# Kernel optimization log

Measured on AMD Instinct MI355X. Metric: run time of the kernel, lower is better.

The kernel has to match this reference:

```python
import jax, jax.numpy as jnp
import numpy as np


def _maxpool3d(x, win):
    # x: (B, C, D, H, W); SAME padding via w//2 on each spatial side, stride 1
    pads = [(0, 0), (0, 0)] + [(w // 2, w // 2) for w in win]
    return jax.lax.reduce_window(x, -jnp.inf, jax.lax.max,
                                 (1, 1) + tuple(win), (1, 1, 1, 1, 1), pads)


def _soft_skeletonize(x, thresh_width=5):
    # Iterative morphological erosion: x <- relu(x - relu(maxpool(minpool(x)) - minpool(x)))
    for _ in range(thresh_width):
        p1 = -_maxpool3d(-x, (3, 1, 1))  # directional min-pool along D
        p2 = -_maxpool3d(-x, (1, 3, 1))  # along H
        p3 = -_maxpool3d(-x, (1, 1, 3))  # along W
        min_pool = jnp.minimum(jnp.minimum(p1, p2), p3)
        contour = jax.nn.relu(_maxpool3d(min_pool, (3, 3, 3)) - min_pool)
        x = jax.nn.relu(x - contour)
    return x


def _positive_intersection(center_line, vessel):
    B, C = center_line.shape[0], center_line.shape[1]
    clf = center_line.reshape(B, C, -1)
    vf = vessel.reshape(B, C, -1)
    intersection = jnp.sum(clf * vf, axis=-1).sum(0)          # (C,)
    return (intersection + 1e-12) / (jnp.sum(clf, axis=-1).sum(0) + 1e-12)


def setup_inputs() -> dict:
    key = jax.random.key(0)
    k1, k2 = jax.random.split(key)
    B, C, D, H, W = 2, 1, 64, 256, 256
    logits = jax.random.normal(k1, (B, C, D, H, W), dtype=jnp.float32)
    target = jax.random.uniform(k2, (B, C, D, H, W), dtype=jnp.float32)
    mask = jnp.ones((B, C, D, H, W), dtype=jnp.float32)
    return {"logits": logits, "target": target, "mask": mask}


def reference(logits, target, mask):
    THRESH_WIDTH = 5
    pred = jax.nn.sigmoid(logits) * mask
    tgt = target * mask
    target_skeleton = _soft_skeletonize(tgt, THRESH_WIDTH)
    cl_pred = _soft_skeletonize(pred, THRESH_WIDTH)
    clrecall = _positive_intersection(target_skeleton, pred)[0]
    clacc = _positive_intersection(cl_pred, tgt)[0]
    cldice = 2.0 * clrecall * clacc / (clrecall + clacc + 1e-12)
    return 1.0 - cldice
```

## Files before the change

kernel.cpp:

```cpp
#include <hip/hip_runtime.h>
#include <math.h>


constexpr int Bn = 2;
constexpr int D  = 64;
constexpr int H  = 256;
constexpr int W  = 256;
constexpr int HW = H * W;
constexpr int NV = Bn * D * H * W;

constexpr int CD  = 16;
constexpr int XSF = 76;
constexpr int XPQ = 768;
constexpr int RSF = 68;

__device__ __forceinline__ void seg_barrier_v0() {
    asm volatile("s_waitcnt vmcnt(0) lgkmcnt(0)" ::: "memory");
    __builtin_amdgcn_s_barrier();
    asm volatile("" ::: "memory");
}
__device__ __forceinline__ void seg_barrier_v2() {
    asm volatile("s_waitcnt vmcnt(2) lgkmcnt(0)" ::: "memory");
    __builtin_amdgcn_s_barrier();
    asm volatile("" ::: "memory");
}

__device__ __forceinline__ float4 vmin4(float4 a, float4 b) {
    return make_float4(fminf(a.x,b.x), fminf(a.y,b.y), fminf(a.z,b.z), fminf(a.w,b.w));
}
__device__ __forceinline__ float4 vmax4(float4 a, float4 b) {
    return make_float4(fmaxf(a.x,b.x), fmaxf(a.y,b.y), fmaxf(a.z,b.z), fmaxf(a.w,b.w));
}
__device__ __forceinline__ float4 sh1(float4 a, float4 b) { return make_float4(a.y,a.z,a.w,b.x); }
__device__ __forceinline__ float4 sh3(float4 a, float4 b) { return make_float4(a.w,b.x,b.y,b.z); }

__global__ __launch_bounds__(256) void prep_kernel(const float* __restrict__ logits,
                                                   const float* __restrict__ target,
                                                   const float* __restrict__ mask,
                                                   float* __restrict__ pred,
                                                   float* __restrict__ tgt,
                                                   float* __restrict__ infbuf) {
    int i = (blockIdx.x * 256 + threadIdx.x) * 4;
    float4 lg = *(const float4*)(logits + i);
    float4 tg = *(const float4*)(target + i);
    float4 mk = *(const float4*)(mask + i);
    float4 p, t;
    p.x = (1.0f/(1.0f+expf(-lg.x)))*mk.x;  t.x = tg.x*mk.x;
    p.y = (1.0f/(1.0f+expf(-lg.y)))*mk.y;  t.y = tg.y*mk.y;
    p.z = (1.0f/(1.0f+expf(-lg.z)))*mk.z;  t.z = tg.z*mk.z;
    p.w = (1.0f/(1.0f+expf(-lg.w)))*mk.w;  t.w = tg.w*mk.w;
    *(float4*)(pred + i) = p;
    *(float4*)(tgt + i)  = t;
    if (blockIdx.x == 0 && threadIdx.x == 0) {
        *(float4*)infbuf = make_float4(INFINITY, INFINITY, INFINITY, INFINITY);
    }
}

template <bool FINAL>
__global__ __launch_bounds__(256) void skel_iter_kernel(
        const float* __restrict__ in0, float* __restrict__ out0,
        const float* __restrict__ oth0, double* __restrict__ acc0,
        const float* __restrict__ in1, float* __restrict__ out1,
        const float* __restrict__ oth1, double* __restrict__ acc1,
        const float* __restrict__ infbuf) {
    __shared__ float sx[4][XPQ * 4];
    __shared__ float srm[2][34 * RSF];

    int cpx = gridDim.x >> 3;
    int hwb = blockIdx.x;
    int bx  = (hwb & 7) * cpx + (hwb >> 3);

    int t   = bx >> 8;
    int bt  = bx & 255;
    int w0  = (bt & 3) * 64;
    int h0  = ((bt >> 2) & 7) * 32;
    int gd0 = ((bt >> 5) & 3) * CD;
    int b   = (bt >> 7) & 1;

    const float* xin  = t ? in1  : in0;
    float*       xout = t ? out1 : out0;
    const float* oth  = t ? oth1 : oth0;
    double*      accp = t ? acc1 : acc0;

    int tid  = threadIdx.x;
    int r    = tid >> 3;
    int k    = tid & 7;
    int wv   = tid >> 6;
    int lane = tid & 63;

    const float* xb  = xin + b * (D * HW);
    float*       ob  = xout ? (xout + b * (D * HW)) : nullptr;
    const float* otb = oth + b * (D * HW);

    const float4 INF4  = make_float4( INFINITY,  INFINITY,  INFINITY,  INFINITY);
    const float4 NINF4 = make_float4(-INFINITY, -INFINITY, -INFINITY, -INFINITY);

    int  offe[3];
    bool okl[3];
    for (int i = 0; i < 3; ++i) {
        int c = wv + 4 * i;
        int j = 64 * c + lane;
        int row = j / 19;
        int q = j - 19 * row;
        int gh = h0 - 2 + row;
        int gw = w0 - 4 + 4 * q;
        okl[i] = (q < 18) && (row < 36) &&
                 ((unsigned)gh < (unsigned)H) && ((unsigned)gw < (unsigned)W);
        offe[i] = gh * W + gw;
    }

    auto issue_g = [&](int p) {
        bool pok = (p >= 0 && p < D);
        const float* pbase = xb + (long)p * HW;
        float* slot = sx[(p + 4) & 3];
        #pragma unroll
        for (int i = 0; i < 3; ++i) {
            const float* src = (pok && okl[i]) ? (pbase + offe[i]) : infbuf;
            float* dst = slot + (wv + 4 * i) * 256;
            __builtin_amdgcn_global_load_lds(
                (const __attribute__((address_space(1))) void*)src,
                (__attribute__((address_space(3))) void*)dst, 16, 0, 0);
        }
    };

    issue_g(gd0 - 2); issue_g(gd0 - 1); issue_g(gd0); issue_g(gd0 + 1);
    __syncthreads();

    float4 h1lo=NINF4, h1hi=NINF4, h2lo=NINF4, h2hi=NINF4;
    float4 p1lo=NINF4, p1hi=NINF4, p2lo=NINF4, p2hi=NINF4;
    float4 rmplo=NINF4, rmphi=NINF4;
    float4 xplo=INF4, xphi=INF4;
    double s0 = 0.0, s1 = 0.0;

    for (int s = gd0 - 1; s <= gd0 + CD + 1; ++s) {
        if (s >= gd0 && s + 2 <= gd0 + CD + 1) issue_g(s + 2);
        asm volatile("" ::: "memory");

        bool sv = (s >= 0 && s < D && s <= gd0 + CD);
        float4 lo = NINF4, hi = NINF4, rmlo = NINF4, rmhi = NINF4;
        float4 vM1 = INF4, vM2 = INF4;
        if (sv) {
            const float* xq = sx[(s + 4) & 3];
            const float* xm = sx[(s + 3) & 3];
            const float* xp = sx[(s + 5) & 3];
            {
                const float* rc  = &xq[(r + 2) * XSF + 8 * k];
                const float* ru  = &xq[(r + 1) * XSF + 8 * k];
                const float* rd  = &xq[(r + 3) * XSF + 8 * k];
                const float* rm_ = &xm[(r + 2) * XSF + 8 * k];
                const float* rp_ = &xp[(r + 2) * XSF + 8 * k];
                float4 X0 = *(const float4*)rc,        X1 = *(const float4*)(rc + 4),
                       X2 = *(const float4*)(rc + 8),  X3 = *(const float4*)(rc + 12);
                float4 U1 = *(const float4*)(ru + 4),  U2 = *(const float4*)(ru + 8);
                float4 Dn1= *(const float4*)(rd + 4),  Dn2= *(const float4*)(rd + 8);
                float4 M1 = *(const float4*)(rm_ + 4), M2 = *(const float4*)(rm_ + 8);
                float4 P1 = *(const float4*)(rp_ + 4), P2 = *(const float4*)(rp_ + 8);
                vM1 = M1; vM2 = M2;
                lo = vmin4(vmin4(sh3(X0, X1), X1), sh1(X1, X2));
                lo = vmin4(lo, vmin4(vmin4(U1, Dn1), vmin4(M1, P1)));
                hi = vmin4(vmin4(sh3(X1, X2), X2), sh1(X2, X3));
                hi = vmin4(hi, vmin4(vmin4(U2, Dn2), vmin4(M2, P2)));
                float eL = __shfl_up(hi.w, 1);
                float eR = __shfl_down(lo.x, 1);
                if (k == 0) {
                    eL = -INFINITY;
                    if (w0 > 0) {
                        float w3 = fminf(fminf(X0.z, X0.w), X1.x);
                        eL = fminf(fminf(w3, fminf(ru[3], rd[3])),
                                   fminf(rm_[3], rp_[3]));
                    }
                }
                if (k == 7) {
                    eR = -INFINITY;
                    if (w0 + 64 < W) {
                        float w3 = fminf(fminf(X2.w, X3.x), X3.y);
                        eR = fminf(fminf(w3, fminf(ru[12], rd[12])),
                                   fminf(rm_[12], rp_[12]));
                    }
                }
                rmlo = vmax4(vmax4(make_float4(eL, lo.x, lo.y, lo.z), lo),
                             make_float4(lo.y, lo.z, lo.w, hi.x));
                rmhi = vmax4(vmax4(make_float4(lo.w, hi.x, hi.y, hi.z), hi),
                             make_float4(hi.y, hi.z, hi.w, eR));
                float* rw = &srm[s & 1][(r + 1) * RSF + 8 * k];
                *(float4*)rw       = rmlo;
                *(float4*)(rw + 4) = rmhi;
            }
            if (tid < 16) {
                int mr2 = (tid >> 3) ? 33 : 0;
                int k2  = tid & 7;
                int gh2 = h0 - 1 + mr2;
                float4 hlo = NINF4, hhi = NINF4;
                if ((unsigned)gh2 < (unsigned)H) {
                    int xr2 = mr2 + 1;
                    const float* rc  = &xq[xr2 * XSF + 8 * k2];
                    const float* ru  = &xq[(xr2 - 1) * XSF + 8 * k2];
                    const float* rd  = &xq[(xr2 + 1) * XSF + 8 * k2];
                    const float* rm_ = &xm[xr2 * XSF + 8 * k2];
                    const float* rp_ = &xp[xr2 * XSF + 8 * k2];
                    float4 X0 = *(const float4*)rc,        X1 = *(const float4*)(rc + 4),
                           X2 = *(const float4*)(rc + 8),  X3 = *(const float4*)(rc + 12);
                    float4 U1 = *(const float4*)(ru + 4),  U2 = *(const float4*)(ru + 8);
                    float4 Dn1= *(const float4*)(rd + 4),  Dn2= *(const float4*)(rd + 8);
                    float4 M1 = *(const float4*)(rm_ + 4), M2 = *(const float4*)(rm_ + 8);
                    float4 P1 = *(const float4*)(rp_ + 4), P2 = *(const float4*)(rp_ + 8);
                    float4 l2 = vmin4(vmin4(sh3(X0, X1), X1), sh1(X1, X2));
                    l2 = vmin4(l2, vmin4(vmin4(U1, Dn1), vmin4(M1, P1)));
                    float4 g2 = vmin4(vmin4(sh3(X1, X2), X2), sh1(X2, X3));
                    g2 = vmin4(g2, vmin4(vmin4(U2, Dn2), vmin4(M2, P2)));
                    float eL2 = -INFINITY, eR2 = -INFINITY;
                    if (w0 + 8 * k2 - 1 >= 0) {
                        float w3 = fminf(fminf(X0.z, X0.w), X1.x);
                        eL2 = fminf(fminf(w3, fminf(ru[3], rd[3])),
                                    fminf(rm_[3], rp_[3]));
                    }
                    if (w0 + 8 * k2 + 8 < W) {
                        float w3 = fminf(fminf(X2.w, X3.x), X3.y);
                        eR2 = fminf(fminf(w3, fminf(ru[12], rd[12])),
                                    fminf(rm_[12], rp_[12]));
                    }
                    hlo = vmax4(vmax4(make_float4(eL2, l2.x, l2.y, l2.z), l2),
                                make_float4(l2.y, l2.z, l2.w, g2.x));
                    hhi = vmax4(vmax4(make_float4(l2.w, g2.x, g2.y, g2.z), g2),
                                make_float4(g2.y, g2.z, g2.w, eR2));
                }
                float* hw = &srm[s & 1][mr2 * RSF + 8 * k2];
                *(float4*)hw       = hlo;
                *(float4*)(hw + 4) = hhi;
            }
        }

        int dm = s - 1;
        float4 xclo = INF4, xchi = INF4;
        if (dm >= gd0 && dm <= gd0 + CD - 1) {
            if (sv) { xclo = vM1; xchi = vM2; }
            else {
                const float* xd = sx[(dm + 4) & 3];
                xclo = *(const float4*)&xd[(r + 2) * XSF + 8 * k + 4];
                xchi = *(const float4*)&xd[(r + 2) * XSF + 8 * k + 8];
            }
        }

        float4 hclo = NINF4, hchi = NINF4;
        if (s >= gd0 && dm >= 0 && dm < D) {
            const float* m = srm[dm & 1];
            float4 a0 = *(const float4*)&m[r * RSF + 8 * k];
            float4 a1 = *(const float4*)&m[r * RSF + 8 * k + 4];
            float4 b0 = *(const float4*)&m[(r + 2) * RSF + 8 * k];
            float4 b1 = *(const float4*)&m[(r + 2) * RSF + 8 * k + 4];
            hclo = vmax4(vmax4(a0, rmplo), b0);
            hchi = vmax4(vmax4(a1, rmphi), b1);
        }

        int d = s - 2;
        if (d >= gd0 && d <= gd0 + CD - 1) {
            float4 mxlo = vmax4(h2lo, vmax4(h1lo, hclo));
            float4 mxhi = vmax4(h2hi, vmax4(h1hi, hchi));
            float4 rlo, rhi;
            rlo.x = fmaxf(xplo.x - (mxlo.x - p2lo.x), 0.0f);
            rlo.y = fmaxf(xplo.y - (mxlo.y - p2lo.y), 0.0f);
            rlo.z = fmaxf(xplo.z - (mxlo.z - p2lo.z), 0.0f);
            rlo.w = fmaxf(xplo.w - (mxlo.w - p2lo.w), 0.0f);
            rhi.x = fmaxf(xphi.x - (mxhi.x - p2hi.x), 0.0f);
            rhi.y = fmaxf(xphi.y - (mxhi.y - p2hi.y), 0.0f);
            rhi.z = fmaxf(xphi.z - (mxhi.z - p2hi.z), 0.0f);
            rhi.w = fmaxf(xphi.w - (mxhi.w - p2hi.w), 0.0f);
            long off = (long)d * HW + (h0 + r) * W + (w0 + 8 * k);
            if constexpr (FINAL) {
                float4 o1 = *(const float4*)(otb + off);
                float4 o2 = *(const float4*)(otb + off + 4);
                s0 += (double)(rlo.x * o1.x) + (double)(rlo.y * o1.y)
                    + (double)(rlo.z * o1.z) + (double)(rlo.w * o1.w)
                    + (double)(rhi.x * o2.x) + (double)(rhi.y * o2.y)
                    + (double)(rhi.z * o2.z) + (double)(rhi.w * o2.w);
                s1 += (double)rlo.x + (double)rlo.y + (double)rlo.z + (double)rlo.w
                    + (double)rhi.x + (double)rhi.y + (double)rhi.z + (double)rhi.w;
            } else {
                *(float4*)(ob + off)     = rlo;
                *(float4*)(ob + off + 4) = rhi;
            }
        }

        h2lo = h1lo; h2hi = h1hi; h1lo = hclo; h1hi = hchi;
        p2lo = p1lo; p2hi = p1hi; p1lo = lo;   p1hi = hi;
        rmplo = rmlo; rmphi = rmhi;
        xplo = xclo;  xphi = xchi;

        if (s <= gd0 + 1) seg_barrier_v0();
        else              seg_barrier_v2();
    }

    if constexpr (FINAL) {
        for (int off = 32; off > 0; off >>= 1) {
            s0 += __shfl_down(s0, off, 64);
            s1 += __shfl_down(s1, off, 64);
        }
        if ((tid & 63) == 0) {
            atomicAdd(&accp[0], s0);
            atomicAdd(&accp[1], s1);
        }
    }
}

__global__ void final_kernel(const double* __restrict__ acc, float* __restrict__ out) {
    double clrecall = (acc[0] + 1e-12) / (acc[1] + 1e-12);
    double clacc    = (acc[2] + 1e-12) / (acc[3] + 1e-12);
    double cldice   = 2.0 * clrecall * clacc / (clrecall + clacc + 1e-12);
    out[0] = (float)(1.0 - cldice);
}

extern "C" void kernel_launch(void* const* d_in, const int* in_sizes, int n_in,
                              void* d_out, int out_size, void* d_ws, size_t ws_size,
                              hipStream_t stream) {
    const float* logits = (const float*)d_in[0];
    const float* target = (const float*)d_in[1];
    const float* mask   = (const float*)d_in[2];
    float* out = (float*)d_out;

    float* pred = (float*)d_ws;
    float* tgt  = pred + NV;
    float* A0   = tgt + NV;
    float* B0   = A0 + NV;

    bool big = ws_size >= (size_t)6 * NV * 4 + 64;
    float* A1    = big ? (B0 + NV) : A0;
    float* B1    = big ? (A1 + NV) : B0;
    double* acc  = big ? (double*)(B1 + NV) : (double*)(B0 + NV);
    float* infb  = (float*)(acc + 4);

    hipMemsetAsync(acc, 0, 4 * sizeof(double), stream);

    dim3 blk(256);
    prep_kernel<<<dim3(NV / 1024), blk, 0, stream>>>(logits, target, mask, pred, tgt, infb);

    if (big) {
        dim3 g(512);
        skel_iter_kernel<false><<<g, blk, 0, stream>>>(tgt, A0, pred, acc, pred, A1, tgt, acc + 2, infb);
        skel_iter_kernel<false><<<g, blk, 0, stream>>>(A0, B0, pred, acc, A1, B1, tgt, acc + 2, infb);
        skel_iter_kernel<false><<<g, blk, 0, stream>>>(B0, A0, pred, acc, B1, A1, tgt, acc + 2, infb);
        skel_iter_kernel<false><<<g, blk, 0, stream>>>(A0, B0, pred, acc, A1, B1, tgt, acc + 2, infb);
        skel_iter_kernel<true ><<<g, blk, 0, stream>>>(B0, nullptr, pred, acc, B1, nullptr, tgt, acc + 2, infb);
    } else {
        dim3 g(256);
        skel_iter_kernel<false><<<g, blk, 0, stream>>>(tgt, A0, pred, acc, tgt, A0, pred, acc, infb);
        skel_iter_kernel<false><<<g, blk, 0, stream>>>(A0, B0, pred, acc, A0, B0, pred, acc, infb);
        skel_iter_kernel<false><<<g, blk, 0, stream>>>(B0, A0, pred, acc, B0, A0, pred, acc, infb);
        skel_iter_kernel<false><<<g, blk, 0, stream>>>(A0, B0, pred, acc, A0, B0, pred, acc, infb);
        skel_iter_kernel<true ><<<g, blk, 0, stream>>>(B0, nullptr, pred, acc, B0, nullptr, pred, acc, infb);
        skel_iter_kernel<false><<<g, blk, 0, stream>>>(pred, A0, tgt, acc + 2, pred, A0, tgt, acc + 2, infb);
        skel_iter_kernel<false><<<g, blk, 0, stream>>>(A0, B0, tgt, acc + 2, A0, B0, tgt, acc + 2, infb);
        skel_iter_kernel<false><<<g, blk, 0, stream>>>(B0, A0, tgt, acc + 2, B0, A0, tgt, acc + 2, infb);
        skel_iter_kernel<false><<<g, blk, 0, stream>>>(A0, B0, tgt, acc + 2, A0, B0, tgt, acc + 2, infb);
        skel_iter_kernel<true ><<<g, blk, 0, stream>>>(B0, nullptr, tgt, acc + 2, B0, nullptr, tgt, acc + 2, infb);
    }

    final_kernel<<<1, 1, 0, stream>>>(acc, out);
}
```

Measured before the change: 282.7 us.

## Fuse sigmoid/mask prep into first and final skeleton iteration kernels

Removes the separate prep kernel and the pred/tgt intermediate buffers. The first skeletonization pass now loads logits/target and mask through registers, applies sigmoid and masking, and writes the result to LDS with a register-prefetch pipeline in place of async global-to-LDS loads. The final pass recomputes pred or tgt on the fly for the intersection sums. This cuts a full read/write sweep of the volume and one launch, but the first pass loses the asynchronous LDS load path and recomputes sigmoid on halo elements.

```diff
diff --git a/kernel.cpp b/kernel.cpp
--- a/kernel.cpp
+++ b/kernel.cpp
@@ -24,6 +24,11 @@
     __builtin_amdgcn_s_barrier();
     asm volatile("" ::: "memory");
 }
+__device__ __forceinline__ void seg_barrier_lgkm() {
+    asm volatile("s_waitcnt lgkmcnt(0)" ::: "memory");
+    __builtin_amdgcn_s_barrier();
+    asm volatile("" ::: "memory");
+}
 
 __device__ __forceinline__ float4 vmin4(float4 a, float4 b) {
     return make_float4(fminf(a.x,b.x), fminf(a.y,b.y), fminf(a.z,b.z), fminf(a.w,b.w));
@@ -34,34 +39,31 @@
 __device__ __forceinline__ float4 sh1(float4 a, float4 b) { return make_float4(a.y,a.z,a.w,b.x); }
 __device__ __forceinline__ float4 sh3(float4 a, float4 b) { return make_float4(a.w,b.x,b.y,b.z); }
 
-__global__ __launch_bounds__(256) void prep_kernel(const float* __restrict__ logits,
-                                                   const float* __restrict__ target,
-                                                   const float* __restrict__ mask,
-                                                   float* __restrict__ pred,
-                                                   float* __restrict__ tgt,
-                                                   float* __restrict__ infbuf) {
-    int i = (blockIdx.x * 256 + threadIdx.x) * 4;
-    float4 lg = *(const float4*)(logits + i);
-    float4 tg = *(const float4*)(target + i);
-    float4 mk = *(const float4*)(mask + i);
-    float4 p, t;
-    p.x = (1.0f/(1.0f+expf(-lg.x)))*mk.x;  t.x = tg.x*mk.x;
-    p.y = (1.0f/(1.0f+expf(-lg.y)))*mk.y;  t.y = tg.y*mk.y;
-    p.z = (1.0f/(1.0f+expf(-lg.z)))*mk.z;  t.z = tg.z*mk.z;
-    p.w = (1.0f/(1.0f+expf(-lg.w)))*mk.w;  t.w = tg.w*mk.w;
-    *(float4*)(pred + i) = p;
-    *(float4*)(tgt + i)  = t;
-    if (blockIdx.x == 0 && threadIdx.x == 0) {
-        *(float4*)infbuf = make_float4(INFINITY, INFINITY, INFINITY, INFINITY);
-    }
-}
-
-template <bool FINAL>
+__device__ __forceinline__ float4 apply_mode(float4 a, const float* __restrict__ pm,
+                                             long ix, int mode) {
+    if (mode != 0) {
+        if (mode == 2) {
+            a.x = 1.0f / (1.0f + expf(-a.x));
+            a.y = 1.0f / (1.0f + expf(-a.y));
+            a.z = 1.0f / (1.0f + expf(-a.z));
+            a.w = 1.0f / (1.0f + expf(-a.w));
+        }
+        float4 m = *(const float4*)(pm + ix);
+        a.x *= m.x; a.y *= m.y; a.z *= m.z; a.w *= m.w;
+    }
+    return a;
+}
+
+template <bool FINAL, int IM0, int IM1, int OM0, int OM1>
 __global__ __launch_bounds__(256) void skel_iter_kernel(
-        const float* __restrict__ in0, float* __restrict__ out0,
-        const float* __restrict__ oth0, double* __restrict__ acc0,
-        const float* __restrict__ in1, float* __restrict__ out1,
-        const float* __restrict__ oth1, double* __restrict__ acc1,
+        const float* __restrict__ iA0, const float* __restrict__ iB0,
+        float* __restrict__ out0,
+        const float* __restrict__ oA0, const float* __restrict__ oB0,
+        double* __restrict__ acc0,
+        const float* __restrict__ iA1, const float* __restrict__ iB1,
+        float* __restrict__ out1,
+        const float* __restrict__ oA1, const float* __restrict__ oB1,
+        double* __restrict__ acc1,
         const float* __restrict__ infbuf) {
     __shared__ float sx[4][XPQ * 4];
     __shared__ float srm[2][34 * RSF];
@@ -77,10 +79,14 @@
     int gd0 = ((bt >> 5) & 3) * CD;
     int b   = (bt >> 7) & 1;
 
-    const float* xin  = t ? in1  : in0;
-    float*       xout = t ? out1 : out0;
-    const float* oth  = t ? oth1 : oth0;
-    double*      accp = t ? acc1 : acc0;
+    const float* iA = t ? iA1 : iA0;
+    const float* iB = t ? iB1 : iB0;
+    const int    im = t ? IM1 : IM0;
+    float*     xout = t ? out1 : out0;
+    const float* oA = t ? oA1 : oA0;
+    const float* oB = t ? oB1 : oB0;
+    const int    om = t ? OM1 : OM0;
+    double*    accp = t ? acc1 : acc0;
 
     int tid  = threadIdx.x;
     int r    = tid >> 3;
@@ -88,9 +94,12 @@
     int wv   = tid >> 6;
     int lane = tid & 63;
 
-    const float* xb  = xin + b * (D * HW);
-    float*       ob  = xout ? (xout + b * (D * HW)) : nullptr;
-    const float* otb = oth + b * (D * HW);
+    long base = (long)b * (D * HW);
+    const float* xbA = iA + base;
+    const float* xbB = iB ? iB + base : nullptr;
+    float*       ob  = xout ? xout + base : nullptr;
+    const float* otA = oA ? oA + base : nullptr;
+    const float* otB = oB ? oB + base : nullptr;
 
     const float4 INF4  = make_float4( INFINITY,  INFINITY,  INFINITY,  INFINITY);
     const float4 NINF4 = make_float4(-INFINITY, -INFINITY, -INFINITY, -INFINITY);
@@ -111,7 +120,7 @@
 
     auto issue_g = [&](int p) {
         bool pok = (p >= 0 && p < D);
-        const float* pbase = xb + (long)p * HW;
+        const float* pbase = xbA + (long)p * HW;
         float* slot = sx[(p + 4) & 3];
         #pragma unroll
         for (int i = 0; i < 3; ++i) {
@@ -123,7 +132,38 @@
         }
     };
 
-    issue_g(gd0 - 2); issue_g(gd0 - 1); issue_g(gd0); issue_g(gd0 + 1);
+    float4 Pa, Pb, Pc;
+    auto issue_r = [&](int p) {
+        if (p < 0 || p >= D) { Pa = Pb = Pc = INF4; return; }
+        const float* pA = xbA + (long)p * HW;
+        const float* pM = xbB ? xbB + (long)p * HW : nullptr;
+        float4 v[3];
+        #pragma unroll
+        for (int i = 0; i < 3; ++i) {
+            if (okl[i]) {
+                float4 a = *(const float4*)(pA + offe[i]);
+                v[i] = apply_mode(a, pM, offe[i], im);
+            } else {
+                v[i] = INF4;
+            }
+        }
+        Pa = v[0]; Pb = v[1]; Pc = v[2];
+    };
+    auto commit_r = [&](int p, float4 va, float4 vb, float4 vc) {
+        float* slot = sx[(p + 4) & 3];
+        *(float4*)&slot[(wv + 0) * 256 + 4 * lane] = va;
+        *(float4*)&slot[(wv + 4) * 256 + 4 * lane] = vb;
+        *(float4*)&slot[(wv + 8) * 256 + 4 * lane] = vc;
+    };
+
+    if constexpr (IM0 >= 0) {
+        issue_r(gd0 - 2); commit_r(gd0 - 2, Pa, Pb, Pc);
+        issue_r(gd0 - 1); commit_r(gd0 - 1, Pa, Pb, Pc);
+        issue_r(gd0);     commit_r(gd0,     Pa, Pb, Pc);
+        issue_r(gd0 + 1);
+    } else {
+        issue_g(gd0 - 2); issue_g(gd0 - 1); issue_g(gd0); issue_g(gd0 + 1);
+    }
     __syncthreads();
 
     float4 h1lo=NINF4, h1hi=NINF4, h2lo=NINF4, h2hi=NINF4;
@@ -133,8 +173,14 @@
     double s0 = 0.0, s1 = 0.0;
 
     for (int s = gd0 - 1; s <= gd0 + CD + 1; ++s) {
-        if (s >= gd0 && s + 2 <= gd0 + CD + 1) issue_g(s + 2);
-        asm volatile("" ::: "memory");
+        if constexpr (IM0 >= 0) {
+            float4 Ta = Pa, Tb = Pb, Tc = Pc;
+            if (s + 3 <= gd0 + CD + 1) issue_r(s + 3);
+            if (s + 2 <= gd0 + CD + 1) commit_r(s + 2, Ta, Tb, Tc);
+        } else {
+            if (s >= gd0 && s + 2 <= gd0 + CD + 1) issue_g(s + 2);
+            asm volatile("" ::: "memory");
+        }
 
         bool sv = (s >= 0 && s < D && s <= gd0 + CD);
         float4 lo = NINF4, hi = NINF4, rmlo = NINF4, rmhi = NINF4;
@@ -267,8 +313,10 @@
             rhi.w = fmaxf(xphi.w - (mxhi.w - p2hi.w), 0.0f);
             long off = (long)d * HW + (h0 + r) * W + (w0 + 8 * k);
             if constexpr (FINAL) {
-                float4 o1 = *(const float4*)(otb + off);
-                float4 o2 = *(const float4*)(otb + off + 4);
+                float4 o1 = *(const float4*)(otA + off);
+                o1 = apply_mode(o1, otB, off, om);
+                float4 o2 = *(const float4*)(otA + off + 4);
+                o2 = apply_mode(o2, otB, off + 4, om);
                 s0 += (double)(rlo.x * o1.x) + (double)(rlo.y * o1.y)
                     + (double)(rlo.z * o1.z) + (double)(rlo.w * o1.w)
                     + (double)(rhi.x * o2.x) + (double)(rhi.y * o2.y)
@@ -286,8 +334,12 @@
         rmplo = rmlo; rmphi = rmhi;
         xplo = xclo;  xphi = xchi;
 
-        if (s <= gd0 + 1) seg_barrier_v0();
-        else              seg_barrier_v2();
+        if constexpr (IM0 >= 0) {
+            seg_barrier_lgkm();
+        } else {
+            if (s <= gd0 + 1) seg_barrier_v0();
+            else              seg_barrier_v2();
+        }
     }
 
     if constexpr (FINAL) {
@@ -316,42 +368,60 @@
     const float* target = (const float*)d_in[1];
     const float* mask   = (const float*)d_in[2];
     float* out = (float*)d_out;
-
-    float* pred = (float*)d_ws;
-    float* tgt  = pred + NV;
-    float* A0   = tgt + NV;
-    float* B0   = A0 + NV;
-
-    bool big = ws_size >= (size_t)6 * NV * 4 + 64;
+    const float* Z = nullptr;
+
+    float* A0 = (float*)d_ws;
+    float* B0 = A0 + NV;
+
+    bool big = ws_size >= (size_t)4 * NV * 4 + 64;
     float* A1    = big ? (B0 + NV) : A0;
     float* B1    = big ? (A1 + NV) : B0;
     double* acc  = big ? (double*)(B1 + NV) : (double*)(B0 + NV);
     float* infb  = (float*)(acc + 4);
 
     hipMemsetAsync(acc, 0, 4 * sizeof(double), stream);
+    hipMemsetAsync(infb, 0x7F, 16, stream);
 
     dim3 blk(256);
-    prep_kernel<<<dim3(NV / 1024), blk, 0, stream>>>(logits, target, mask, pred, tgt, infb);
 
     if (big) {
         dim3 g(512);
-        skel_iter_kernel<false><<<g, blk, 0, stream>>>(tgt, A0, pred, acc, pred, A1, tgt, acc + 2, infb);
-        skel_iter_kernel<false><<<g, blk, 0, stream>>>(A0, B0, pred, acc, A1, B1, tgt, acc + 2, infb);
-        skel_iter_kernel<false><<<g, blk, 0, stream>>>(B0, A0, pred, acc, B1, A1, tgt, acc + 2, infb);
-        skel_iter_kernel<false><<<g, blk, 0, stream>>>(A0, B0, pred, acc, A1, B1, tgt, acc + 2, infb);
-        skel_iter_kernel<true ><<<g, blk, 0, stream>>>(B0, nullptr, pred, acc, B1, nullptr, tgt, acc + 2, infb);
+        skel_iter_kernel<false, 1, 2, 0, 0><<<g, blk, 0, stream>>>(
+            target, mask, A0, Z, Z, acc,
+            logits, mask, A1, Z, Z, acc + 2, infb);
+        skel_iter_kernel<false, -1, -1, 0, 0><<<g, blk, 0, stream>>>(
+            A0, Z, B0, Z, Z, acc,  A1, Z, B1, Z, Z, acc + 2, infb);
+        skel_iter_kernel<false, -1, -1, 0, 0><<<g, blk, 0, stream>>>(
+            B0, Z, A0, Z, Z, acc,  B1, Z, A1, Z, Z, acc + 2, infb);
+        skel_iter_kernel<false, -1, -1, 0, 0><<<g, blk, 0, stream>>>(
+            A0, Z, B0, Z, Z, acc,  A1, Z, B1, Z, Z, acc + 2, infb);
+        skel_iter_kernel<true, -1, -1, 2, 1><<<g, blk, 0, stream>>>(
+            B0, Z, nullptr, logits, mask, acc,
+            B1, Z, nullptr, target, mask, acc + 2, infb);
     } else {
         dim3 g(256);
-        skel_iter_kernel<false><<<g, blk, 0, stream>>>(tgt, A0, pred, acc, tgt, A0, pred, acc, infb);
-        skel_iter_kernel<false><<<g, blk, 0, stream>>>(A0, B0, pred, acc, A0, B0, pred, acc, infb);
-        skel_iter_kernel<false><<<g, blk, 0, stream>>>(B0, A0, pred, acc, B0, A0, pred, acc, infb);
-        skel_iter_kernel<false><<<g, blk, 0, stream>>>(A0, B0, pred, acc, A0, B0, pred, acc, infb);
-        skel_iter_kernel<true ><<<g, blk, 0, stream>>>(B0, nullptr, pred, acc, B0, nullptr, pred, acc, infb);
-        skel_iter_kernel<false><<<g, blk, 0, stream>>>(pred, A0, tgt, acc + 2, pred, A0, tgt, acc + 2, infb);
-        skel_iter_kernel<false><<<g, blk, 0, stream>>>(A0, B0, tgt, acc + 2, A0, B0, tgt, acc + 2, infb);
-        skel_iter_kernel<false><<<g, blk, 0, stream>>>(B0, A0, tgt, acc + 2, B0, A0, tgt, acc + 2, infb);
-        skel_iter_kernel<false><<<g, blk, 0, stream>>>(A0, B0, tgt, acc + 2, A0, B0, tgt, acc + 2, infb);
-        skel_iter_kernel<true ><<<g, blk, 0, stream>>>(B0, nullptr, tgt, acc + 2, B0, nullptr, tgt, acc + 2, infb);
+        skel_iter_kernel<false, 1, 1, 0, 0><<<g, blk, 0, stream>>>(
+            target, mask, A0, Z, Z, acc,  target, mask, A0, Z, Z, acc, infb);
+        skel_iter_kernel<false, -1, -1, 0, 0><<<g, blk, 0, stream>>>(
+            A0, Z, B0, Z, Z, acc,  A0, Z, B0, Z, Z, acc, infb);
+        skel_iter_kernel<false, -1, -1, 0, 0><<<g, blk, 0, stream>>>(
+            B0, Z, A0, Z, Z, acc,  B0, Z, A0, Z, Z, acc, infb);
+        skel_iter_kernel<false, -1, -1, 0, 0><<<g, blk, 0, stream>>>(
+            A0, Z, B0, Z, Z, acc,  A0, Z, B0, Z, Z, acc, infb);
+        skel_iter_kernel<true, -1, -1, 2, 2><<<g, blk, 0, stream>>>(
+            B0, Z, nullptr, logits, mask, acc,
+            B0, Z, nullptr, logits, mask, acc, infb);
+        skel_iter_kernel<false, 2, 2, 0, 0><<<g, blk, 0, stream>>>(
+            logits, mask, A0, Z, Z, acc + 2,  logits, mask, A0, Z, Z, acc + 2, infb);
+        skel_iter_kernel<false, -1, -1, 0, 0><<<g, blk, 0, stream>>>(
+            A0, Z, B0, Z, Z, acc + 2,  A0, Z, B0, Z, Z, acc + 2, infb);
+        skel_iter_kernel<false, -1, -1, 0, 0><<<g, blk, 0, stream>>>(
+            B0, Z, A0, Z, Z, acc + 2,  B0, Z, A0, Z, Z, acc + 2, infb);
+        skel_iter_kernel<false, -1, -1, 0, 0><<<g, blk, 0, stream>>>(
+            A0, Z, B0, Z, Z, acc + 2,  A0, Z, B0, Z, Z, acc + 2, infb);
+        skel_iter_kernel<true, -1, -1, 1, 1><<<g, blk, 0, stream>>>(
+            B0, Z, nullptr, target, mask, acc + 2,
+            B0, Z, nullptr, target, mask, acc + 2, infb);
     }
 
     final_kernel<<<1, 1, 0, stream>>>(acc, out);
```

After: 312.9 us. 10.7% more time.
